# Performance work log

Measured on AMD Instinct MI355X. Metric: run time of the kernel, lower is better.

Reference implementation:

```python
import jax, jax.numpy as jnp
import numpy as np

B, N, DIM = 8, 4096, 1024
H, DH = 16, 64          # heads, dim_head -> inner_dim = 1024
P = 256                 # proj_size (Linformer low-rank seq projection)
SCALE = DH ** -0.5


def setup_inputs() -> dict:
    key = jax.random.key(0)
    ks = jax.random.split(key, 6)
    return {
        "x": jax.random.normal(ks[0], (B, N, DIM), dtype=jnp.float32),
        "Wqkv": jax.random.normal(ks[1], (3 * H * DH, DIM), dtype=jnp.float32) * 0.02,
        "We": jax.random.normal(ks[2], (P, N), dtype=jnp.float32) * 0.02,
        "be": jax.random.normal(ks[3], (P,), dtype=jnp.float32) * 0.02,
        "Wo": jax.random.normal(ks[4], (DIM, H * DH), dtype=jnp.float32) * 0.02,
        "bo": jax.random.normal(ks[5], (DIM,), dtype=jnp.float32) * 0.02,
    }


def reference(x, Wqkv, We, be, Wo, bo):
    b, n, _ = x.shape
    # fused QKV projection (no bias), split, reshape to (b, h, n, d)
    qkv = jnp.einsum('bnc,ec->bne', x, Wqkv)                      # [b, n, 3*h*d]
    q, k, v = jnp.split(qkv, 3, axis=-1)
    tohead = lambda t: t.reshape(b, n, H, DH).transpose(0, 2, 1, 3)
    q, k, v = tohead(q), tohead(k), tohead(v)
    # shared E=F sequence projection: Linear over seq axis n -> p, bias along p
    kp = jnp.einsum('bhnd,pn->bhpd', k, We) + be[None, None, :, None]
    vp = jnp.einsum('bhnd,pn->bhpd', v, We) + be[None, None, :, None]
    dots = jnp.einsum('bhid,bhjd->bhij', q, kp) * SCALE           # [b, h, n, p]
    attn = jax.nn.softmax(dots, axis=-1)
    out = jnp.einsum('bhij,bhjd->bhid', attn, vp)                 # [b, h, n, d]
    out = out.transpose(0, 2, 1, 3).reshape(b, n, H * DH)
    return jnp.einsum('bne,oe->bno', out, Wo) + bo                # [b, n, dim]
```

## Files before the change

### kernel.cpp

```cpp
#include <hip/hip_runtime.h>
#include <hip/hip_bf16.h>


typedef unsigned short bf16u;
typedef __attribute__((ext_vector_type(8))) short short8;
typedef __attribute__((ext_vector_type(4))) float f32x4;

__device__ __forceinline__ unsigned short f2bf(float f) {
    unsigned u = __float_as_uint(f);
    u += 0x7FFF + ((u >> 16) & 1);
    return (unsigned short)(u >> 16);
}

__device__ __forceinline__ f32x4 mfma16(short8 a, short8 b, f32x4 c) {
    return __builtin_amdgcn_mfma_f32_16x16x32_bf16(a, b, c, 0, 0, 0);
}

#define AS1 __attribute__((address_space(1)))
#define AS3 __attribute__((address_space(3)))

__global__ void cvt_kernel(const float* __restrict__ in, bf16u* __restrict__ out, int n4) {
    int i = blockIdx.x * blockDim.x + threadIdx.x;
    int stride = gridDim.x * blockDim.x;
    for (int j = i; j < n4; j += stride) {
        float4 v = ((const float4*)in)[j];
        union { bf16u s[4]; uint2 u; } o;
        o.s[0] = f2bf(v.x); o.s[1] = f2bf(v.y); o.s[2] = f2bf(v.z); o.s[3] = f2bf(v.w);
        ((uint2*)out)[j] = o.u;
    }
}

__global__ __launch_bounds__(256) void cvt_transpose_x(const float* __restrict__ x,
                                                       bf16u* __restrict__ Xbf,
                                                       bf16u* __restrict__ XT) {
    __shared__ bf16u T[64][72];
    const int b = blockIdx.z;
    const int n0 = blockIdx.y * 64, c0 = blockIdx.x * 64;
    const int t = threadIdx.x;
    const int cx = t & 15, ry = t >> 4;
#pragma unroll
    for (int p = 0; p < 4; p++) {
        const int nn = p * 16 + ry;
        const size_t g = ((size_t)b * 4096 + n0 + nn) * 1024 + c0 + cx * 4;
        float4 v = *(const float4*)&x[g];
        union { bf16u s[4]; uint2 u; } o;
        o.s[0] = f2bf(v.x); o.s[1] = f2bf(v.y); o.s[2] = f2bf(v.z); o.s[3] = f2bf(v.w);
        *(uint2*)&Xbf[g] = o.u;
#pragma unroll
        for (int j = 0; j < 4; j++) T[cx * 4 + j][nn] = o.s[j];
    }
    __syncthreads();
    const int cc = t >> 2, ch = t & 3;
#pragma unroll
    for (int j = 0; j < 2; j++) {
        const int nch = ch + j * 4;
        short8 vv = *(const short8*)&T[cc][nch * 8];
        *(short8*)&XT[((size_t)b * 1024 + c0 + cc) * 4096 + n0 + nch * 8] = vv;
    }
}

__device__ __forceinline__ void gemm_core_128(const bf16u* __restrict__ Ablk, int ldA,
                                              const bf16u* __restrict__ Bblk, int ldB,
                                              int Kiter, f32x4 (&acc)[4][4]) {
    __shared__ __align__(16) bf16u As[128 * 32];
    __shared__ __align__(16) bf16u Bs[128 * 32];
    const int t = threadIdx.x;
    const int wave = t >> 6, lane = t & 63;
    const int wm = (wave >> 1) * 64, wn = (wave & 1) * 64;
    const int lr = lane & 15, lk = (lane >> 4) * 8;

    for (int kt = 0; kt < Kiter; kt += 32) {
#pragma unroll
        for (int i = 0; i < 2; i++) {
            int c = i * 256 + wave * 64 + lane;
            const bf16u* ga = Ablk + (size_t)(c >> 2) * ldA + kt + (c & 3) * 8;
            const bf16u* gb = Bblk + (size_t)(c >> 2) * ldB + kt + (c & 3) * 8;
            __builtin_amdgcn_global_load_lds((const AS1 unsigned*)ga,
                (AS3 unsigned*)(&As[(i * 256 + wave * 64) * 8]), 16, 0, 0);
            __builtin_amdgcn_global_load_lds((const AS1 unsigned*)gb,
                (AS3 unsigned*)(&Bs[(i * 256 + wave * 64) * 8]), 16, 0, 0);
        }
        __syncthreads();
        short8 a[4], b[4];
#pragma unroll
        for (int mi = 0; mi < 4; mi++)
            a[mi] = *(const short8*)&As[(wm + mi * 16 + lr) * 32 + lk];
#pragma unroll
        for (int ni = 0; ni < 4; ni++)
            b[ni] = *(const short8*)&Bs[(wn + ni * 16 + lr) * 32 + lk];
#pragma unroll
        for (int mi = 0; mi < 4; mi++)
#pragma unroll
            for (int ni = 0; ni < 4; ni++)
                acc[mi][ni] = mfma16(a[mi], b[ni], acc[mi][ni]);
        __syncthreads();
    }
}

__global__ __launch_bounds__(256) void gemm_ex_splitk(const bf16u* __restrict__ We,
                                                      const bf16u* __restrict__ XT,
                                                      float* __restrict__ Cpart) {
    const int bn = blockIdx.x, bm = blockIdx.y;
    const int bz = blockIdx.z >> 2, ks = blockIdx.z & 3;
    f32x4 acc[4][4];
#pragma unroll
    for (int i = 0; i < 4; i++)
#pragma unroll
        for (int j = 0; j < 4; j++) acc[i][j] = f32x4{0.f, 0.f, 0.f, 0.f};

    gemm_core_128(We + (size_t)bm * 128 * 4096 + ks * 1024, 4096,
                  XT + ((size_t)bz * 1024 + bn * 128) * 4096 + ks * 1024, 4096,
                  1024, acc);

    const int lane = threadIdx.x & 63, wave = threadIdx.x >> 6;
    const int wm = (wave >> 1) * 64, wn = (wave & 1) * 64;
    const int lr = lane & 15, lg = (lane >> 4) * 4;
    float* Cp = Cpart + (size_t)(ks * 8 + bz) * 256 * 1024;
#pragma unroll
    for (int ni = 0; ni < 4; ni++) {
        const int col = bn * 128 + wn + ni * 16 + lr;
#pragma unroll
        for (int mi = 0; mi < 4; mi++) {
#pragma unroll
            for (int r = 0; r < 4; r++) {
                const int row = bm * 128 + wm + mi * 16 + lg + r;
                Cp[(size_t)row * 1024 + col] = acc[mi][ni][r];
            }
        }
    }
}

__global__ __launch_bounds__(256) void reduce4_cvt(const float* __restrict__ P,
                                                   bf16u* __restrict__ out) {
    const int j = blockIdx.x * blockDim.x + threadIdx.x;
    const float4* p = (const float4*)P;
    float4 s0 = p[j], s1 = p[j + 524288], s2 = p[j + 1048576], s3 = p[j + 1572864];
    union { bf16u s[4]; uint2 u; } o;
    o.s[0] = f2bf((s0.x + s1.x) + (s2.x + s3.x));
    o.s[1] = f2bf((s0.y + s1.y) + (s2.y + s3.y));
    o.s[2] = f2bf((s0.z + s1.z) + (s2.z + s3.z));
    o.s[3] = f2bf((s0.w + s1.w) + (s2.w + s3.w));
    ((uint2*)out)[j] = o.u;
}

__global__ __launch_bounds__(256) void gemm_kpv(const bf16u* __restrict__ EX,
                                                const bf16u* __restrict__ Wkv,
                                                const float* __restrict__ be,
                                                bf16u* __restrict__ kp,
                                                bf16u* __restrict__ vpT) {
    const int bn = blockIdx.x, bm = blockIdx.y, bz = blockIdx.z;
    f32x4 acc[4][4];
#pragma unroll
    for (int i = 0; i < 4; i++)
#pragma unroll
        for (int j = 0; j < 4; j++) acc[i][j] = f32x4{0.f, 0.f, 0.f, 0.f};

    gemm_core_128(EX + (size_t)bz * 256 * 1024 + (size_t)bm * 128 * 1024, 1024,
                  Wkv + (size_t)bn * 128 * 1024, 1024, 1024, acc);

    const int lane = threadIdx.x & 63, wave = threadIdx.x >> 6;
    const int wm = (wave >> 1) * 64, wn = (wave & 1) * 64;
    const int lr = lane & 15, lg = (lane >> 4) * 4;
    bf16u* kpB = kp + (size_t)bz * 256 * 1024;
    bf16u* vpB = vpT + (size_t)bz * 1024 * 256;
    const int ebase = bn * 128 + wn;
#pragma unroll
    for (int ni = 0; ni < 4; ni++) {
        const int col = ebase + ni * 16 + lr;
        const int region = (ebase + ni * 16) >> 10;
#pragma unroll
        for (int mi = 0; mi < 4; mi++) {
            const int p0 = bm * 128 + wm + mi * 16 + lg;
            if (region == 0) {
#pragma unroll
                for (int r = 0; r < 4; r++)
                    kpB[(size_t)(p0 + r) * 1024 + col] = f2bf(acc[mi][ni][r] + be[p0 + r]);
            } else {
                const int d = col - 1024;
                union { bf16u s[4]; uint2 u; } o;
#pragma unroll
                for (int r = 0; r < 4; r++) o.s[r] = f2bf(acc[mi][ni][r] + be[p0 + r]);
                *(uint2*)&vpB[(size_t)d * 256 + p0] = o.u;
            }
        }
    }
}

template<int MODE>
__global__ __launch_bounds__(512, 2) void gemm8p(const bf16u* __restrict__ A,
                                                 const bf16u* __restrict__ Bt,
                                                 const float* __restrict__ bias,
                                                 void* __restrict__ Cout,
                                                 int K) {
    __shared__ __align__(16) bf16u L[2][32768];

    const int nwg = gridDim.x;
    const int bid = blockIdx.x;
    const int logical = (bid & 7) * (nwg >> 3) + (bid >> 3);
    const int bn = logical & 3, bm = logical >> 2;

    const bf16u* Ablk = A + (size_t)bm * 256 * K;
    const bf16u* Bblk = Bt + (size_t)bn * 256 * K;

    const int t = threadIdx.x;
    const int wid = t >> 6, lane = t & 63;
    const int wm = (wid >> 2) * 128, wn = (wid & 3) * 64;
    const int lr = lane & 15, g4 = lane >> 4;

    f32x4 acc[8][4];
#pragma unroll
    for (int i = 0; i < 8; i++)
#pragma unroll
        for (int j = 0; j < 4; j++) acc[i][j] = f32x4{0.f, 0.f, 0.f, 0.f};

    auto STAGE = [&](int buf, int which, int half, int kt) {
#pragma unroll
        for (int i = 0; i < 2; i++) {
            const int c = i * 512 + t;
            const int row = half * 128 + (c >> 3);
            const int gp = c & 7;
            const int col = kt * 64 + ((gp ^ (row & 7)) << 3);
            const bf16u* src = (which ? Bblk : Ablk) + (size_t)row * K + col;
            __builtin_amdgcn_global_load_lds((const AS1 unsigned*)src,
                (AS3 unsigned*)(&L[buf][which * 16384 + half * 8192 + c * 8]), 16, 0, 0);
        }
    };

    short8 aF[4][2], bE[2][2], bO[2][2];
    auto LDA = [&](int buf, int mq) {
#pragma unroll
        for (int mi = 0; mi < 4; mi++) {
            const int row = wm + mq * 64 + mi * 16 + lr;
#pragma unroll
            for (int ks = 0; ks < 2; ks++) {
                const int gp = (ks * 4 + g4) ^ (row & 7);
                aF[mi][ks] = *(const short8*)&L[buf][row * 64 + gp * 8];
            }
        }
    };
    auto LDB = [&](int buf, int nq, short8 (&bF)[2][2]) {
#pragma unroll
        for (int ni = 0; ni < 2; ni++) {
            const int row = wn + nq * 32 + ni * 16 + lr;
#pragma unroll
            for (int ks = 0; ks < 2; ks++) {
                const int gp = (ks * 4 + g4) ^ (row & 7);
                bF[ni][ks] = *(const short8*)&L[buf][16384 + row * 64 + gp * 8];
            }
        }
    };
    auto MM = [&](int mq, int nq, short8 (&bF)[2][2]) {
        __builtin_amdgcn_s_setprio(1);
#pragma unroll
        for (int mi = 0; mi < 4; mi++)
#pragma unroll
            for (int nj = 0; nj < 2; nj++)
#pragma unroll
                for (int ks = 0; ks < 2; ks++)
                    acc[mq * 4 + mi][nq * 2 + nj] =
                        mfma16(aF[mi][ks], bF[nj][ks], acc[mq * 4 + mi][nq * 2 + nj]);
        __builtin_amdgcn_s_setprio(0);
    };
    auto BAR = [&]() {
        asm volatile("" ::: "memory");
        __builtin_amdgcn_s_barrier();
        asm volatile("" ::: "memory");
    };
    auto LGKM0 = [&]() {
        asm volatile("s_waitcnt lgkmcnt(0)" ::: "memory");
        __builtin_amdgcn_sched_barrier(0);
    };

    const int nkt = K >> 6;
    const int niter = nkt >> 1;

    STAGE(0, 0, 0, 0); STAGE(0, 0, 1, 0); STAGE(0, 1, 0, 0); STAGE(0, 1, 1, 0);
    STAGE(1, 0, 0, 1); STAGE(1, 0, 1, 1); STAGE(1, 1, 0, 1); STAGE(1, 1, 1, 1);
    asm volatile("s_waitcnt vmcnt(8)" ::: "memory");
    BAR();

    for (int it = 0; it < niter; it++) {
        const int kt1 = 2 * it + 1, kt2 = 2 * it + 2, kt3 = 2 * it + 3;
        const bool p123 = (it > 0), s4 = (kt2 < nkt), s8 = (kt3 < nkt);

        LDA(0, 0); LDB(0, 0, bE);
        if (p123) STAGE(1, 0, 1, kt1);
        asm volatile("s_waitcnt lgkmcnt(8)" ::: "memory");
        BAR(); LGKM0();
        MM(0, 0, bE);
        BAR();
        LDB(0, 1, bO);
        if (p123) STAGE(1, 1, 0, kt1);
        BAR(); LGKM0();
        MM(0, 1, bO);
        BAR();
        LDA(0, 1);
        if (p123) STAGE(1, 1, 1, kt1);
        BAR(); LGKM0();
        MM(1, 1, bO);
        BAR();
        if (s4) STAGE(0, 0, 0, kt2);
        MM(1, 0, bE);
        if (s4) asm volatile("s_waitcnt vmcnt(2)" ::: "memory");
        else    asm volatile("s_waitcnt vmcnt(0)" ::: "memory");
        BAR();

        LDA(1, 0); LDB(1, 0, bE);
        if (s4) STAGE(0, 0, 1, kt2);
        asm volatile("s_waitcnt lgkmcnt(8)" ::: "memory");
        BAR(); LGKM0();
        MM(0, 0, bE);
        BAR();
        LDB(1, 1, bO);
        if (s4) STAGE(0, 1, 0, kt2);
        BAR(); LGKM0();
        MM(0, 1, bO);
        BAR();
        LDA(1, 1);
        if (s4) STAGE(0, 1, 1, kt2);
        BAR(); LGKM0();
        MM(1, 1, bO);
        BAR();
        if (s8) STAGE(1, 0, 0, kt3);
        MM(1, 0, bE);
        if (s8) asm volatile("s_waitcnt vmcnt(2)" ::: "memory");
        else    asm volatile("s_waitcnt vmcnt(0)" ::: "memory");
        BAR();
    }

    const int lg = g4 * 4;
    if (MODE == 0) {
        bf16u* C = (bf16u*)Cout;
#pragma unroll
        for (int mi = 0; mi < 8; mi++) {
#pragma unroll
            for (int r = 0; r < 4; r++) {
                const size_t row = (size_t)bm * 256 + wm + mi * 16 + lg + r;
#pragma unroll
                for (int ni = 0; ni < 4; ni++)
                    C[row * 1024 + bn * 256 + wn + ni * 16 + lr] = f2bf(acc[mi][ni][r]);
            }
        }
    } else {
        float* C = (float*)Cout;
        float bv[4];
#pragma unroll
        for (int ni = 0; ni < 4; ni++) bv[ni] = bias[bn * 256 + wn + ni * 16 + lr];
#pragma unroll
        for (int mi = 0; mi < 8; mi++) {
#pragma unroll
            for (int r = 0; r < 4; r++) {
                const size_t row = (size_t)bm * 256 + wm + mi * 16 + lg + r;
#pragma unroll
                for (int ni = 0; ni < 4; ni++)
                    C[row * 1024 + bn * 256 + wn + ni * 16 + lr] = acc[mi][ni][r] + bv[ni];
            }
        }
    }
}

__global__ __launch_bounds__(256, 2) void attn_kernel(const bf16u* __restrict__ Q,
                                                      const bf16u* __restrict__ kp,
                                                      const bf16u* __restrict__ vpT,
                                                      bf16u* __restrict__ O) {
    __shared__ __align__(16) bf16u S[32768];
    const int bh = blockIdx.y, b = bh >> 4, h = bh & 15;
    const int t = threadIdx.x;
    const int wave = t >> 6, lane = t & 63;
    const int lr = lane & 15, g = lane >> 4;
    const int i0 = blockIdx.x * 128 + wave * 16;
    const size_t mrow = (size_t)b * 4096 + i0;

    short8 bq0[2], bq1[2];
    const bf16u* Qb0 = Q + (mrow + lr) * 1024 + h * 64 + g * 8;
    bq0[0] = *(const short8*)&Qb0[0];
    bq0[1] = *(const short8*)&Qb0[32];
    const bf16u* Qb1 = Qb0 + (size_t)64 * 1024;
    bq1[0] = *(const short8*)&Qb1[0];
    bq1[1] = *(const short8*)&Qb1[32];

    const bf16u* kpb = kp + ((size_t)b * 256) * 1024 + h * 64;
    const bf16u* vpb = vpT + ((size_t)b * 1024 + h * 64) * 256;
#pragma unroll
    for (int i = 0; i < 8; i++) {
        const int c = i * 256 + t;
        const int ubase = (i * 256 + wave * 64) * 8;
        {
            const int p = c >> 3, d8 = (c & 7) ^ (p & 7);
            __builtin_amdgcn_global_load_lds(
                (const AS1 unsigned*)(kpb + (size_t)p * 1024 + d8 * 8),
                (AS3 unsigned*)&S[ubase], 16, 0, 0);
        }
        {
            const int d = c >> 5, p8 = (c & 31) ^ (d & 15);
            __builtin_amdgcn_global_load_lds(
                (const AS1 unsigned*)(vpb + (size_t)d * 256 + p8 * 8),
                (AS3 unsigned*)&S[16384 + ubase], 16, 0, 0);
        }
    }
    __syncthreads();

    f32x4 d0[16], d1[16];
#pragma unroll
    for (int pj = 0; pj < 16; pj++) { d0[pj] = f32x4{0.f,0.f,0.f,0.f}; d1[pj] = f32x4{0.f,0.f,0.f,0.f}; }
    __builtin_amdgcn_s_setprio(1);
#pragma unroll
    for (int pj = 0; pj < 16; pj++) {
#pragma unroll
        for (int kk = 0; kk < 2; kk++) {
            const int gr = (pj * 16 + lr) * 8 + ((kk * 4 + g) ^ (lr & 7));
            short8 ak = *(const short8*)&S[gr * 8];
            d0[pj] = mfma16(ak, bq0[kk], d0[pj]);
            d1[pj] = mfma16(ak, bq1[kk], d1[pj]);
        }
    }
    __builtin_amdgcn_s_setprio(0);

    float s0 = 0.f;
#pragma unroll
    for (int pj = 0; pj < 16; pj++) {
#pragma unroll
        for (int r = 0; r < 4; r++) {
            float e = __expf(d0[pj][r] * 0.125f);
            d0[pj][r] = e;
            s0 += e;
        }
    }
    s0 += __shfl_xor(s0, 16);
    s0 += __shfl_xor(s0, 32);
    const float inv0 = 1.0f / s0;
    float invO0[4];
#pragma unroll
    for (int r = 0; r < 4; r++) invO0[r] = __shfl(inv0, g * 4 + r);

    unsigned pkw0[16][2];
#pragma unroll
    for (int pj = 0; pj < 16; pj++) {
        asm("v_cvt_pk_bf16_f32 %0, %1, %2" : "=v"(pkw0[pj][0]) : "v"(d0[pj][0]), "v"(d0[pj][1]));
        asm("v_cvt_pk_bf16_f32 %0, %1, %2" : "=v"(pkw0[pj][1]) : "v"(d0[pj][2]), "v"(d0[pj][3]));
    }

    __syncthreads();

    const int pbase = wave * 4096 + lr * 256;
    const int pxor = (lr & 7) << 3;
#pragma unroll
    for (int pj = 0; pj < 16; pj++) {
        const int el = (pbase + pj * 16 + g * 4) ^ pxor;
        uint2 u; u.x = pkw0[pj][0]; u.y = pkw0[pj][1];
        *(uint2*)&S[el] = u;
    }

    float s1 = 0.f;
#pragma unroll
    for (int pj = 0; pj < 16; pj++) {
#pragma unroll
        for (int r = 0; r < 4; r++) {
            float e = __expf(d1[pj][r] * 0.125f);
            d1[pj][r] = e;
            s1 += e;
        }
    }
    s1 += __shfl_xor(s1, 16);
    s1 += __shfl_xor(s1, 32);
    const float inv1 = 1.0f / s1;
    float invO1[4];
#pragma unroll
    for (int r = 0; r < 4; r++) invO1[r] = __shfl(inv1, g * 4 + r);
    unsigned pkw1[16][2];
#pragma unroll
    for (int pj = 0; pj < 16; pj++) {
        asm("v_cvt_pk_bf16_f32 %0, %1, %2" : "=v"(pkw1[pj][0]) : "v"(d1[pj][0]), "v"(d1[pj][1]));
        asm("v_cvt_pk_bf16_f32 %0, %1, %2" : "=v"(pkw1[pj][1]) : "v"(d1[pj][2]), "v"(d1[pj][3]));
    }

    f32x4 oacc0[4];
#pragma unroll
    for (int dj = 0; dj < 4; dj++) oacc0[dj] = f32x4{0.f, 0.f, 0.f, 0.f};
    __builtin_amdgcn_s_setprio(1);
#pragma unroll
    for (int pk = 0; pk < 8; pk++) {
        const int el = (pbase + pk * 32 + g * 8) ^ pxor;
        short8 ap = *(const short8*)&S[el];
#pragma unroll
        for (int dj = 0; dj < 4; dj++) {
            const int d = dj * 16 + lr;
            const int gr = d * 32 + ((pk * 4 + g) ^ (d & 15));
            short8 bv = *(const short8*)&S[16384 + gr * 8];
            oacc0[dj] = mfma16(ap, bv, oacc0[dj]);
        }
    }
    __builtin_amdgcn_s_setprio(0);

#pragma unroll
    for (int pj = 0; pj < 16; pj++) {
        const int el = (pbase + pj * 16 + g * 4) ^ pxor;
        uint2 u; u.x = pkw1[pj][0]; u.y = pkw1[pj][1];
        *(uint2*)&S[el] = u;
    }

    f32x4 oacc1[4];
#pragma unroll
    for (int dj = 0; dj < 4; dj++) oacc1[dj] = f32x4{0.f, 0.f, 0.f, 0.f};
    __builtin_amdgcn_s_setprio(1);
#pragma unroll
    for (int pk = 0; pk < 8; pk++) {
        const int el = (pbase + pk * 32 + g * 8) ^ pxor;
        short8 ap = *(const short8*)&S[el];
#pragma unroll
        for (int dj = 0; dj < 4; dj++) {
            const int d = dj * 16 + lr;
            const int gr = d * 32 + ((pk * 4 + g) ^ (d & 15));
            short8 bv = *(const short8*)&S[16384 + gr * 8];
            oacc1[dj] = mfma16(ap, bv, oacc1[dj]);
        }
    }
    __builtin_amdgcn_s_setprio(0);

    bf16u* Ob0 = O + (mrow + g * 4) * 1024 + h * 64 + lr;
#pragma unroll
    for (int dj = 0; dj < 4; dj++)
#pragma unroll
        for (int r = 0; r < 4; r++)
            Ob0[(size_t)r * 1024 + dj * 16] = f2bf(oacc0[dj][r] * invO0[r]);
    bf16u* Ob1 = Ob0 + (size_t)64 * 1024;
#pragma unroll
    for (int dj = 0; dj < 4; dj++)
#pragma unroll
        for (int r = 0; r < 4; r++)
            Ob1[(size_t)r * 1024 + dj * 16] = f2bf(oacc1[dj][r] * invO1[r]);
}

extern "C" void kernel_launch(void* const* d_in, const int* in_sizes, int n_in,
                              void* d_out, int out_size, void* d_ws, size_t ws_size,
                              hipStream_t stream) {
    const float* x    = (const float*)d_in[0];
    const float* Wqkv = (const float*)d_in[1];
    const float* We   = (const float*)d_in[2];
    const float* be   = (const float*)d_in[3];
    const float* Wo   = (const float*)d_in[4];
    const float* bo   = (const float*)d_in[5];
    float* out = (float*)d_out;

    char* w = (char*)d_ws;
    bf16u* Qbf  = (bf16u*)(w);
    bf16u* Obuf = (bf16u*)(w + 67108864ull);
    bf16u* Wqb  = (bf16u*)(w + 134217728ull);
    bf16u* Web  = (bf16u*)(w + 140509184ull);
    bf16u* Wob  = (bf16u*)(w + 142606336ull);
    bf16u* EXb  = (bf16u*)(w + 144703488ull);
    if (ws_size < 148897792ull) return;

    bf16u* Xbf = (bf16u*)d_out;
    bf16u* XT  = Xbf + 33554432ull;
    float* EXpart = (float*)d_out;
    bf16u* kpb = Xbf;
    bf16u* vpb = Xbf + 2097152ull;

    cvt_transpose_x<<<dim3(16, 64, 8), 256, 0, stream>>>(x, Xbf, XT);
    cvt_kernel<<<768, 256, 0, stream>>>(Wqkv, Wqb, 3145728 / 4);
    cvt_kernel<<<256, 256, 0, stream>>>(We,   Web, 1048576 / 4);
    cvt_kernel<<<256, 256, 0, stream>>>(Wo,   Wob, 1048576 / 4);

    gemm8p<0><<<512, 512, 0, stream>>>(Xbf, Wqb, nullptr, Qbf, 1024);
    gemm_ex_splitk<<<dim3(8, 2, 32), 256, 0, stream>>>(Web, XT, EXpart);
    reduce4_cvt<<<2048, 256, 0, stream>>>(EXpart, EXb);
    gemm_kpv<<<dim3(16, 2, 8), 256, 0, stream>>>(EXb, Wqb + (size_t)1024 * 1024, be, kpb, vpb);

    attn_kernel<<<dim3(32, 128), 256, 0, stream>>>(Qbf, kpb, vpb, Obuf);
    gemm8p<1><<<512, 512, 0, stream>>>(Obuf, Wob, bo, out, 1024);
}
```

Before: 347.3 us.

## Replace 256x256 GEMM with 256x128 tile triple-buffered K=32 pipeline

The Q-projection and output-projection GEMMs switch from a 256x256 tile with a hand-scheduled double-buffered K=64 pipeline to a 256x128 tile with a simpler triple-buffered K=32 loop. Shared memory per block drops and launch bounds rise to 4 blocks per CU, and the grid doubles to 1024 blocks, for more occupancy and better latency hiding. The trade-off is lower arithmetic intensity per tile, more barriers per unit of work, and more global re-reads of the A operand.

```diff
diff --git a/kernel.cpp b/kernel.cpp
--- a/kernel.cpp
+++ b/kernel.cpp
@@ -187,173 +187,128 @@
 }
 
 template<int MODE>
-__global__ __launch_bounds__(512, 2) void gemm8p(const bf16u* __restrict__ A,
-                                                 const bf16u* __restrict__ Bt,
-                                                 const float* __restrict__ bias,
-                                                 void* __restrict__ Cout,
-                                                 int K) {
-    __shared__ __align__(16) bf16u L[2][32768];
+__global__ __launch_bounds__(512, 4) void gemm_p3(const bf16u* __restrict__ A,
+                                                  const bf16u* __restrict__ Bt,
+                                                  const float* __restrict__ bias,
+                                                  void* __restrict__ Cout,
+                                                  int K) {
+    __shared__ __align__(16) bf16u L[3][12288];
 
     const int nwg = gridDim.x;
     const int bid = blockIdx.x;
     const int logical = (bid & 7) * (nwg >> 3) + (bid >> 3);
-    const int bn = logical & 3, bm = logical >> 2;
+    const int bn = logical & 7, bm = logical >> 3;
 
     const bf16u* Ablk = A + (size_t)bm * 256 * K;
-    const bf16u* Bblk = Bt + (size_t)bn * 256 * K;
+    const bf16u* Bblk = Bt + (size_t)bn * 128 * K;
 
     const int t = threadIdx.x;
     const int wid = t >> 6, lane = t & 63;
-    const int wm = (wid >> 2) * 128, wn = (wid & 3) * 64;
+    const int wm = (wid >> 1) * 64, wn = (wid & 1) * 64;
     const int lr = lane & 15, g4 = lane >> 4;
 
-    f32x4 acc[8][4];
-#pragma unroll
-    for (int i = 0; i < 8; i++)
+    f32x4 acc[4][4];
+#pragma unroll
+    for (int i = 0; i < 4; i++)
 #pragma unroll
         for (int j = 0; j < 4; j++) acc[i][j] = f32x4{0.f, 0.f, 0.f, 0.f};
 
-    auto STAGE = [&](int buf, int which, int half, int kt) {
+    auto STAGE = [&](int buf, int kt) {
 #pragma unroll
         for (int i = 0; i < 2; i++) {
             const int c = i * 512 + t;
-            const int row = half * 128 + (c >> 3);
-            const int gp = c & 7;
-            const int col = kt * 64 + ((gp ^ (row & 7)) << 3);
-            const bf16u* src = (which ? Bblk : Ablk) + (size_t)row * K + col;
-            __builtin_amdgcn_global_load_lds((const AS1 unsigned*)src,
-                (AS3 unsigned*)(&L[buf][which * 16384 + half * 8192 + c * 8]), 16, 0, 0);
+            const int row = c >> 2, gp = c & 3;
+            const int col = kt * 32 + ((gp ^ (row & 3)) << 3);
+            __builtin_amdgcn_global_load_lds(
+                (const AS1 unsigned*)(Ablk + (size_t)row * K + col),
+                (AS3 unsigned*)(&L[buf][c * 8]), 16, 0, 0);
+        }
+        {
+            const int c = t;
+            const int row = c >> 2, gp = c & 3;
+            const int col = kt * 32 + ((gp ^ (row & 3)) << 3);
+            __builtin_amdgcn_global_load_lds(
+                (const AS1 unsigned*)(Bblk + (size_t)row * K + col),
+                (AS3 unsigned*)(&L[buf][8192 + c * 8]), 16, 0, 0);
         }
     };
 
-    short8 aF[4][2], bE[2][2], bO[2][2];
-    auto LDA = [&](int buf, int mq) {
-#pragma unroll
-        for (int mi = 0; mi < 4; mi++) {
-            const int row = wm + mq * 64 + mi * 16 + lr;
-#pragma unroll
-            for (int ks = 0; ks < 2; ks++) {
-                const int gp = (ks * 4 + g4) ^ (row & 7);
-                aF[mi][ks] = *(const short8*)&L[buf][row * 64 + gp * 8];
-            }
-        }
-    };
-    auto LDB = [&](int buf, int nq, short8 (&bF)[2][2]) {
-#pragma unroll
-        for (int ni = 0; ni < 2; ni++) {
-            const int row = wn + nq * 32 + ni * 16 + lr;
-#pragma unroll
-            for (int ks = 0; ks < 2; ks++) {
-                const int gp = (ks * 4 + g4) ^ (row & 7);
-                bF[ni][ks] = *(const short8*)&L[buf][16384 + row * 64 + gp * 8];
-            }
-        }
-    };
-    auto MM = [&](int mq, int nq, short8 (&bF)[2][2]) {
-        __builtin_amdgcn_s_setprio(1);
-#pragma unroll
-        for (int mi = 0; mi < 4; mi++)
-#pragma unroll
-            for (int nj = 0; nj < 2; nj++)
-#pragma unroll
-                for (int ks = 0; ks < 2; ks++)
-                    acc[mq * 4 + mi][nq * 2 + nj] =
-                        mfma16(aF[mi][ks], bF[nj][ks], acc[mq * 4 + mi][nq * 2 + nj]);
-        __builtin_amdgcn_s_setprio(0);
-    };
     auto BAR = [&]() {
         asm volatile("" ::: "memory");
         __builtin_amdgcn_s_barrier();
         asm volatile("" ::: "memory");
     };
-    auto LGKM0 = [&]() {
+
+    const int nkt = K >> 5;
+
+    STAGE(0, 0); STAGE(1, 1);
+    asm volatile("s_waitcnt vmcnt(3)" ::: "memory");
+    BAR();
+
+    int cur = 0;
+    for (int p = 0; p < nkt; p++) {
+        const int sbuf = (cur + 2 >= 3) ? cur - 1 : cur + 2;
+
+        short8 a[4], b[4];
+#pragma unroll
+        for (int mi = 0; mi < 4; mi++) {
+            const int row = wm + mi * 16 + lr;
+            const int gp = g4 ^ (row & 3);
+            a[mi] = *(const short8*)&L[cur][row * 32 + gp * 8];
+        }
+#pragma unroll
+        for (int ni = 0; ni < 4; ni++) {
+            const int row = wn + ni * 16 + lr;
+            const int gp = g4 ^ (row & 3);
+            b[ni] = *(const short8*)&L[cur][8192 + row * 32 + gp * 8];
+        }
+        if (p + 2 < nkt) STAGE(sbuf, p + 2);
+
+        BAR();
         asm volatile("s_waitcnt lgkmcnt(0)" ::: "memory");
         __builtin_amdgcn_sched_barrier(0);
-    };
-
-    const int nkt = K >> 6;
-    const int niter = nkt >> 1;
-
-    STAGE(0, 0, 0, 0); STAGE(0, 0, 1, 0); STAGE(0, 1, 0, 0); STAGE(0, 1, 1, 0);
-    STAGE(1, 0, 0, 1); STAGE(1, 0, 1, 1); STAGE(1, 1, 0, 1); STAGE(1, 1, 1, 1);
-    asm volatile("s_waitcnt vmcnt(8)" ::: "memory");
-    BAR();
-
-    for (int it = 0; it < niter; it++) {
-        const int kt1 = 2 * it + 1, kt2 = 2 * it + 2, kt3 = 2 * it + 3;
-        const bool p123 = (it > 0), s4 = (kt2 < nkt), s8 = (kt3 < nkt);
-
-        LDA(0, 0); LDB(0, 0, bE);
-        if (p123) STAGE(1, 0, 1, kt1);
-        asm volatile("s_waitcnt lgkmcnt(8)" ::: "memory");
-        BAR(); LGKM0();
-        MM(0, 0, bE);
+
+        __builtin_amdgcn_s_setprio(1);
+#pragma unroll
+        for (int mi = 0; mi < 4; mi++)
+#pragma unroll
+            for (int ni = 0; ni < 4; ni++)
+                acc[mi][ni] = mfma16(a[mi], b[ni], acc[mi][ni]);
+        __builtin_amdgcn_s_setprio(0);
+
+        if (p + 2 < nkt)      asm volatile("s_waitcnt vmcnt(3)" ::: "memory");
+        else if (p + 1 < nkt) asm volatile("s_waitcnt vmcnt(0)" ::: "memory");
         BAR();
-        LDB(0, 1, bO);
-        if (p123) STAGE(1, 1, 0, kt1);
-        BAR(); LGKM0();
-        MM(0, 1, bO);
-        BAR();
-        LDA(0, 1);
-        if (p123) STAGE(1, 1, 1, kt1);
-        BAR(); LGKM0();
-        MM(1, 1, bO);
-        BAR();
-        if (s4) STAGE(0, 0, 0, kt2);
-        MM(1, 0, bE);
-        if (s4) asm volatile("s_waitcnt vmcnt(2)" ::: "memory");
-        else    asm volatile("s_waitcnt vmcnt(0)" ::: "memory");
-        BAR();
-
-        LDA(1, 0); LDB(1, 0, bE);
-        if (s4) STAGE(0, 0, 1, kt2);
-        asm volatile("s_waitcnt lgkmcnt(8)" ::: "memory");
-        BAR(); LGKM0();
-        MM(0, 0, bE);
-        BAR();
-        LDB(1, 1, bO);
-        if (s4) STAGE(0, 1, 0, kt2);
-        BAR(); LGKM0();
-        MM(0, 1, bO);
-        BAR();
-        LDA(1, 1);
-        if (s4) STAGE(0, 1, 1, kt2);
-        BAR(); LGKM0();
-        MM(1, 1, bO);
-        BAR();
-        if (s8) STAGE(1, 0, 0, kt3);
-        MM(1, 0, bE);
-        if (s8) asm volatile("s_waitcnt vmcnt(2)" ::: "memory");
-        else    asm volatile("s_waitcnt vmcnt(0)" ::: "memory");
-        BAR();
+
+        cur = (cur == 2) ? 0 : cur + 1;
     }
 
     const int lg = g4 * 4;
     if (MODE == 0) {
         bf16u* C = (bf16u*)Cout;
 #pragma unroll
-        for (int mi = 0; mi < 8; mi++) {
+        for (int mi = 0; mi < 4; mi++) {
 #pragma unroll
             for (int r = 0; r < 4; r++) {
                 const size_t row = (size_t)bm * 256 + wm + mi * 16 + lg + r;
 #pragma unroll
                 for (int ni = 0; ni < 4; ni++)
-                    C[row * 1024 + bn * 256 + wn + ni * 16 + lr] = f2bf(acc[mi][ni][r]);
+                    C[row * 1024 + bn * 128 + wn + ni * 16 + lr] = f2bf(acc[mi][ni][r]);
             }
         }
     } else {
         float* C = (float*)Cout;
         float bv[4];
 #pragma unroll
-        for (int ni = 0; ni < 4; ni++) bv[ni] = bias[bn * 256 + wn + ni * 16 + lr];
-#pragma unroll
-        for (int mi = 0; mi < 8; mi++) {
+        for (int ni = 0; ni < 4; ni++) bv[ni] = bias[bn * 128 + wn + ni * 16 + lr];
+#pragma unroll
+        for (int mi = 0; mi < 4; mi++) {
 #pragma unroll
             for (int r = 0; r < 4; r++) {
                 const size_t row = (size_t)bm * 256 + wm + mi * 16 + lg + r;
 #pragma unroll
                 for (int ni = 0; ni < 4; ni++)
-                    C[row * 1024 + bn * 256 + wn + ni * 16 + lr] = acc[mi][ni][r] + bv[ni];
+                    C[row * 1024 + bn * 128 + wn + ni * 16 + lr] = acc[mi][ni][r] + bv[ni];
             }
         }
     }
@@ -562,11 +517,11 @@
     cvt_kernel<<<256, 256, 0, stream>>>(We,   Web, 1048576 / 4);
     cvt_kernel<<<256, 256, 0, stream>>>(Wo,   Wob, 1048576 / 4);
 
-    gemm8p<0><<<512, 512, 0, stream>>>(Xbf, Wqb, nullptr, Qbf, 1024);
+    gemm_p3<0><<<1024, 512, 0, stream>>>(Xbf, Wqb, nullptr, Qbf, 1024);
     gemm_ex_splitk<<<dim3(8, 2, 32), 256, 0, stream>>>(Web, XT, EXpart);
     reduce4_cvt<<<2048, 256, 0, stream>>>(EXpart, EXb);
     gemm_kpv<<<dim3(16, 2, 8), 256, 0, stream>>>(EXb, Wqb + (size_t)1024 * 1024, be, kpb, vpb);
 
     attn_kernel<<<dim3(32, 128), 256, 0, stream>>>(Qbf, kpb, vpb, Obuf);
-    gemm8p<1><<<512, 512, 0, stream>>>(Obuf, Wob, bo, out, 1024);
-}
+    gemm_p3<1><<<1024, 512, 0, stream>>>(Obuf, Wob, bo, out, 1024);
+}
```

After: 339.4 us. 1.02x faster.

## Double-buffer LDS with BK=64 and XOR swizzle in shared GEMM core

Applied to the files above, without the earlier changes.

Replaces the single-buffered 128x128x32 GEMM core with a double-buffered version using a K tile of 64. Loads for the next tile are issued before the current tile's MFMAs, so there is one barrier per iteration instead of two. An XOR swizzle on the LDS layout avoids bank conflicts on the fragment reads. Launch bounds now request 2 blocks per SM. In exchange, LDS use per block grows to 64 KB, which may limit occupancy, and register pressure rises from holding twice as many fragments.

```diff
diff --git a/kernel.cpp b/kernel.cpp
--- a/kernel.cpp
+++ b/kernel.cpp
@@ -59,47 +59,70 @@
     }
 }
 
-__device__ __forceinline__ void gemm_core_128(const bf16u* __restrict__ Ablk, int ldA,
-                                              const bf16u* __restrict__ Bblk, int ldB,
-                                              int Kiter, f32x4 (&acc)[4][4]) {
-    __shared__ __align__(16) bf16u As[128 * 32];
-    __shared__ __align__(16) bf16u Bs[128 * 32];
+__device__ __forceinline__ void gemm_core2(const bf16u* __restrict__ Ablk, int ldA,
+                                           const bf16u* __restrict__ Bblk, int ldB,
+                                           int Kiter, f32x4 (&acc)[4][4]) {
+    __shared__ __align__(16) bf16u As[2][8192];
+    __shared__ __align__(16) bf16u Bs[2][8192];
     const int t = threadIdx.x;
     const int wave = t >> 6, lane = t & 63;
     const int wm = (wave >> 1) * 64, wn = (wave & 1) * 64;
-    const int lr = lane & 15, lk = (lane >> 4) * 8;
-
-    for (int kt = 0; kt < Kiter; kt += 32) {
-#pragma unroll
-        for (int i = 0; i < 2; i++) {
-            int c = i * 256 + wave * 64 + lane;
-            const bf16u* ga = Ablk + (size_t)(c >> 2) * ldA + kt + (c & 3) * 8;
-            const bf16u* gb = Bblk + (size_t)(c >> 2) * ldB + kt + (c & 3) * 8;
-            __builtin_amdgcn_global_load_lds((const AS1 unsigned*)ga,
-                (AS3 unsigned*)(&As[(i * 256 + wave * 64) * 8]), 16, 0, 0);
-            __builtin_amdgcn_global_load_lds((const AS1 unsigned*)gb,
-                (AS3 unsigned*)(&Bs[(i * 256 + wave * 64) * 8]), 16, 0, 0);
-        }
+    const int lr = lane & 15, g4 = lane >> 4;
+
+    auto STAGE = [&](int buf, int kt) {
+#pragma unroll
+        for (int i = 0; i < 4; i++) {
+            const int c = i * 256 + t;
+            const int row = c >> 3, gp = c & 7;
+            const int col = kt * 64 + ((gp ^ (row & 7)) << 3);
+            __builtin_amdgcn_global_load_lds(
+                (const AS1 unsigned*)(Ablk + (size_t)row * ldA + col),
+                (AS3 unsigned*)(&As[buf][c * 8]), 16, 0, 0);
+            __builtin_amdgcn_global_load_lds(
+                (const AS1 unsigned*)(Bblk + (size_t)row * ldB + col),
+                (AS3 unsigned*)(&Bs[buf][c * 8]), 16, 0, 0);
+        }
+    };
+
+    const int nkt = Kiter >> 6;
+    STAGE(0, 0);
+    __syncthreads();
+    for (int kt = 0; kt < nkt; kt++) {
+        const int buf = kt & 1;
+        if (kt + 1 < nkt) STAGE(buf ^ 1, kt + 1);
+        short8 a[4][2], b[4][2];
+#pragma unroll
+        for (int mi = 0; mi < 4; mi++) {
+            const int row = wm + mi * 16 + lr;
+#pragma unroll
+            for (int ks = 0; ks < 2; ks++) {
+                const int gp = (ks * 4 + g4) ^ (row & 7);
+                a[mi][ks] = *(const short8*)&As[buf][row * 64 + gp * 8];
+            }
+        }
+#pragma unroll
+        for (int ni = 0; ni < 4; ni++) {
+            const int row = wn + ni * 16 + lr;
+#pragma unroll
+            for (int ks = 0; ks < 2; ks++) {
+                const int gp = (ks * 4 + g4) ^ (row & 7);
+                b[ni][ks] = *(const short8*)&Bs[buf][row * 64 + gp * 8];
+            }
+        }
+#pragma unroll
+        for (int ks = 0; ks < 2; ks++)
+#pragma unroll
+            for (int mi = 0; mi < 4; mi++)
+#pragma unroll
+                for (int ni = 0; ni < 4; ni++)
+                    acc[mi][ni] = mfma16(a[mi][ks], b[ni][ks], acc[mi][ni]);
         __syncthreads();
-        short8 a[4], b[4];
-#pragma unroll
-        for (int mi = 0; mi < 4; mi++)
-            a[mi] = *(const short8*)&As[(wm + mi * 16 + lr) * 32 + lk];
-#pragma unroll
-        for (int ni = 0; ni < 4; ni++)
-            b[ni] = *(const short8*)&Bs[(wn + ni * 16 + lr) * 32 + lk];
-#pragma unroll
-        for (int mi = 0; mi < 4; mi++)
-#pragma unroll
-            for (int ni = 0; ni < 4; ni++)
-                acc[mi][ni] = mfma16(a[mi], b[ni], acc[mi][ni]);
-        __syncthreads();
-    }
-}
-
-__global__ __launch_bounds__(256) void gemm_ex_splitk(const bf16u* __restrict__ We,
-                                                      const bf16u* __restrict__ XT,
-                                                      float* __restrict__ Cpart) {
+    }
+}
+
+__global__ __launch_bounds__(256, 2) void gemm_ex_splitk(const bf16u* __restrict__ We,
+                                                         const bf16u* __restrict__ XT,
+                                                         float* __restrict__ Cpart) {
     const int bn = blockIdx.x, bm = blockIdx.y;
     const int bz = blockIdx.z >> 2, ks = blockIdx.z & 3;
     f32x4 acc[4][4];
@@ -108,9 +131,9 @@
 #pragma unroll
         for (int j = 0; j < 4; j++) acc[i][j] = f32x4{0.f, 0.f, 0.f, 0.f};
 
-    gemm_core_128(We + (size_t)bm * 128 * 4096 + ks * 1024, 4096,
-                  XT + ((size_t)bz * 1024 + bn * 128) * 4096 + ks * 1024, 4096,
-                  1024, acc);
+    gemm_core2(We + (size_t)bm * 128 * 4096 + ks * 1024, 4096,
+               XT + ((size_t)bz * 1024 + bn * 128) * 4096 + ks * 1024, 4096,
+               1024, acc);
 
     const int lane = threadIdx.x & 63, wave = threadIdx.x >> 6;
     const int wm = (wave >> 1) * 64, wn = (wave & 1) * 64;
@@ -143,11 +166,11 @@
     ((uint2*)out)[j] = o.u;
 }
 
-__global__ __launch_bounds__(256) void gemm_kpv(const bf16u* __restrict__ EX,
-                                                const bf16u* __restrict__ Wkv,
-                                                const float* __restrict__ be,
-                                                bf16u* __restrict__ kp,
-                                                bf16u* __restrict__ vpT) {
+__global__ __launch_bounds__(256, 2) void gemm_kpv(const bf16u* __restrict__ EX,
+                                                   const bf16u* __restrict__ Wkv,
+                                                   const float* __restrict__ be,
+                                                   bf16u* __restrict__ kp,
+                                                   bf16u* __restrict__ vpT) {
     const int bn = blockIdx.x, bm = blockIdx.y, bz = blockIdx.z;
     f32x4 acc[4][4];
 #pragma unroll
@@ -155,8 +178,8 @@
 #pragma unroll
         for (int j = 0; j < 4; j++) acc[i][j] = f32x4{0.f, 0.f, 0.f, 0.f};
 
-    gemm_core_128(EX + (size_t)bz * 256 * 1024 + (size_t)bm * 128 * 1024, 1024,
-                  Wkv + (size_t)bn * 128 * 1024, 1024, 1024, acc);
+    gemm_core2(EX + (size_t)bz * 256 * 1024 + (size_t)bm * 128 * 1024, 1024,
+               Wkv + (size_t)bn * 128 * 1024, 1024, 1024, acc);
 
     const int lane = threadIdx.x & 63, wave = threadIdx.x >> 6;
     const int wm = (wave >> 1) * 64, wn = (wave & 1) * 64;
```

Measured after the change: 341.8 us. About the same (-1.6%).
